# Performance work log

Measured on AMD Instinct MI355X. Metric: run time of the kernel, lower is better.

## Reference

```python
import jax, jax.numpy as jnp
import numpy as np
from math import sqrt

B, S, D, H = 4, 2048, 1024, 16
DH = D // H          # 64
DF = 4 * D           # 4096
EPS = 1e-5
NEG = -1e9


def layer_norm(x, w, b):
    mu = jnp.mean(x, axis=-1, keepdims=True)
    var = jnp.mean((x - mu) ** 2, axis=-1, keepdims=True)
    return (x - mu) * jax.lax.rsqrt(var + EPS) * w + b


def setup_inputs() -> dict:
    key = jax.random.key(0)
    ks = jax.random.split(key, 16)
    s = 0.02
    return {
        "state": jax.random.normal(ks[0], (B, S, D), jnp.float32),
        "mask": jax.random.randint(ks[1], (B, S), 0, 2, jnp.int32),
        "ln1_w": jnp.ones((D,), jnp.float32),
        "ln1_b": jnp.zeros((D,), jnp.float32),
        "Wq": jax.random.normal(ks[2], (H, D, DH), jnp.float32) * s,
        "bq": jnp.zeros((H, DH), jnp.float32),
        "Wk": jax.random.normal(ks[3], (H, D, DH), jnp.float32) * s,
        "bk": jnp.zeros((H, DH), jnp.float32),
        "Wv": jax.random.normal(ks[4], (H, D, DH), jnp.float32) * s,
        "bv": jnp.zeros((H, DH), jnp.float32),
        "Wo": jax.random.normal(ks[5], (D, D), jnp.float32) * s,
        "bo": jnp.zeros((D,), jnp.float32),
        "ln2_w": jnp.ones((D,), jnp.float32),
        "ln2_b": jnp.zeros((D,), jnp.float32),
        "W1": jax.random.normal(ks[6], (D, DF), jnp.float32) * s,
        "b1": jnp.zeros((DF,), jnp.float32),
        "W2": jax.random.normal(ks[7], (DF, D), jnp.float32) * s,
        "b2": jnp.zeros((D,), jnp.float32),
    }


def reference(state, mask, ln1_w, ln1_b, Wq, bq, Wk, bk, Wv, bv, Wo, bo,
              ln2_w, ln2_b, W1, b1, W2, b2):
    # pre-norm attention block
    hidden = layer_norm(state, ln1_w, ln1_b)               # [B,S,D]
    q = jnp.einsum("bsd,hde->bhse", hidden, Wq) + bq[None, :, None, :]
    k = jnp.einsum("bsd,hde->bhse", hidden, Wk) + bk[None, :, None, :]
    v = jnp.einsum("bsd,hde->bhse", hidden, Wv) + bv[None, :, None, :]
    scores = jnp.einsum("bhse,bhte->bhst", q, k) / sqrt(DH)  # [B,H,S,S]
    scores = jnp.where(mask[:, None, None, :] == 0, NEG, scores)
    weights = jax.nn.softmax(scores, axis=-1)
    attended = jnp.einsum("bhst,bhte->bhse", weights, v)    # [B,H,S,DH]
    # concat heads in head order (matches torch cat over per-head outputs)
    attended = attended.transpose(0, 2, 1, 3).reshape(B, S, D)
    attn_out = attended @ Wo + bo
    output = state + attn_out
    # pre-norm FFN block (dropout=0 -> identity)
    hidden = layer_norm(output, ln2_w, ln2_b)
    ff = jax.nn.gelu(hidden @ W1 + b1, approximate=False) @ W2 + b2
    return output + ff
```

## Files before the change

### kernel.cpp

```cpp
#include <hip/hip_runtime.h>
#include <math.h>

#define B_  4
#define S_  2048
#define D_  1024
#define H_  16
#define DH_ 64
#define DF_ 4096
#define M_  8192

#define QSC 0.18033688011112042f

typedef __attribute__((ext_vector_type(8))) short bf8_t;
typedef __attribute__((ext_vector_type(4))) float f4_t;

__device__ __forceinline__ unsigned short f2bf(float x) {
  union { float f; unsigned u; } v; v.f = x;
  unsigned r = v.u + 0x7fffu + ((v.u >> 16) & 1u);
  return (unsigned short)(r >> 16);
}

#if defined(__has_builtin)
#if __has_builtin(__builtin_amdgcn_cvt_pk_bf16_f32)
#define HAVE_PKCVT 1
#endif
#if __has_builtin(__builtin_amdgcn_global_load_lds)
#define HAVE_ASYNC 1
#endif
#endif

__device__ __forceinline__ unsigned pk_bf16(float lo, float hi) {
#ifdef HAVE_PKCVT
  auto r = __builtin_amdgcn_cvt_pk_bf16_f32(lo, hi);
  unsigned u; __builtin_memcpy(&u, &r, 4); return u;
#else
  return (unsigned)f2bf(lo) | ((unsigned)f2bf(hi) << 16);
#endif
}

__device__ __forceinline__ bf8_t upk8(unsigned u0, unsigned u1, unsigned u2, unsigned u3) {
  union { unsigned u[4]; bf8_t v; } c;
  c.u[0] = u0; c.u[1] = u1; c.u[2] = u2; c.u[3] = u3; return c.v;
}

__device__ __forceinline__ f4_t mfma32(bf8_t a, bf8_t b, f4_t c) {
  return __builtin_amdgcn_mfma_f32_16x16x32_bf16(a, b, c, 0, 0, 0);
}

__device__ __forceinline__ void async16(const void* g, void* l) {
#ifdef HAVE_ASYNC
  __builtin_amdgcn_global_load_lds((__attribute__((address_space(1))) void*)(g),
                                   (__attribute__((address_space(3))) void*)(l), 16, 0, 0);
#else
  *(uint4*)l = *(const uint4*)g;
#endif
}

__device__ __forceinline__ int sw(int row) { return (row ^ (row >> 3)) & 7; }


__global__ __launch_bounds__(256) void wtrans_kernel(const float* __restrict__ in,
                                                     unsigned short* __restrict__ out,
                                                     int K, int N) {
  const int k0 = blockIdx.x * 32, n0 = blockIdx.y * 32;
  __shared__ float t[32][33];
  const int tid = threadIdx.x;
#pragma unroll
  for (int i = 0; i < 4; i++) {
    int idx = i * 256 + tid; int r = idx >> 5, c = idx & 31;
    t[r][c] = in[(size_t)(k0 + r) * N + n0 + c];
  }
  __syncthreads();
#pragma unroll
  for (int i = 0; i < 4; i++) {
    int idx = i * 256 + tid; int r = idx >> 5, c = idx & 31;
    out[(size_t)(n0 + r) * K + k0 + c] = f2bf(t[c][r]);
  }
}

__global__ __launch_bounds__(256) void qkvpack_kernel(const float* __restrict__ Wq,
                                                      const float* __restrict__ Wk,
                                                      const float* __restrict__ Wv,
                                                      unsigned short* __restrict__ WqkvT) {
  const int z = blockIdx.z;
  const int sel = z >> 4, h = z & 15;
  const float* in = (sel == 0 ? Wq : sel == 1 ? Wk : Wv) + (size_t)h * D_ * DH_;
  const int k0 = blockIdx.x * 32, n0 = blockIdx.y * 32;
  __shared__ float t[32][33];
  const int tid = threadIdx.x;
#pragma unroll
  for (int i = 0; i < 4; i++) {
    int idx = i * 256 + tid; int r = idx >> 5, c = idx & 31;
    t[r][c] = in[(size_t)(k0 + r) * DH_ + n0 + c];
  }
  __syncthreads();
#pragma unroll
  for (int i = 0; i < 4; i++) {
    int idx = i * 256 + tid; int r = idx >> 5, c = idx & 31;
    int n = sel * 1024 + h * 64 + n0 + r;
    WqkvT[(size_t)n * D_ + k0 + c] = f2bf(t[c][r]);
  }
}

__global__ void biaspack_kernel(const float* __restrict__ bq, const float* __restrict__ bk,
                                const float* __restrict__ bv, float* __restrict__ bqkv) {
  int i = blockIdx.x * 256 + threadIdx.x;
  if (i < 3072) {
    int sel = i >> 10, j = i & 1023;
    const float* src = sel == 0 ? bq : sel == 1 ? bk : bv;
    bqkv[i] = src[j];
  }
}


__global__ __launch_bounds__(256) void ln_kernel(const float* __restrict__ x,
                                                 const float* __restrict__ w,
                                                 const float* __restrict__ bb,
                                                 unsigned short* __restrict__ out) {
  const int row = blockIdx.x;
  const float* xr = x + (size_t)row * D_;
  const int tid = threadIdx.x;
  float v[4]; float s = 0.f;
#pragma unroll
  for (int i = 0; i < 4; i++) { v[i] = xr[tid + i * 256]; s += v[i]; }
  __shared__ float red[8];
#pragma unroll
  for (int o = 32; o; o >>= 1) s += __shfl_xor(s, o, 64);
  const int wv = tid >> 6, ln = tid & 63;
  if (!ln) red[wv] = s;
  __syncthreads();
  float mean = (red[0] + red[1] + red[2] + red[3]) * (1.f / 1024.f);
  float s2 = 0.f;
#pragma unroll
  for (int i = 0; i < 4; i++) { float d = v[i] - mean; s2 += d * d; }
#pragma unroll
  for (int o = 32; o; o >>= 1) s2 += __shfl_xor(s2, o, 64);
  if (!ln) red[4 + wv] = s2;
  __syncthreads();
  float var = (red[4] + red[5] + red[6] + red[7]) * (1.f / 1024.f);
  float rstd = rsqrtf(var + 1e-5f);
#pragma unroll
  for (int i = 0; i < 4; i++) {
    int c = tid + i * 256;
    out[(size_t)row * D_ + c] = f2bf((v[i] - mean) * rstd * w[c] + bb[c]);
  }
}

template <int EPI>
__global__ __launch_bounds__(256) void gemm_bt(const unsigned short* __restrict__ A,
                                               const unsigned short* __restrict__ Bt,
                                               const float* __restrict__ bias,
                                               const float* __restrict__ resid,
                                               unsigned short* __restrict__ outb,
                                               float* __restrict__ outf,
                                               int Ndim, int Kdim) {
  __shared__ __align__(16) unsigned short Asmem[4096];
  __shared__ __align__(16) unsigned short Bsmem[4096];
  const int tid = threadIdx.x;
  const int wave = tid >> 6, lane = tid & 63;
  const int quad = lane >> 4, l16 = lane & 15;
  const int wm = wave >> 1, wn = wave & 1;
  const int m0 = blockIdx.y * 128, n0 = blockIdx.x * 128;

  const f4_t fzero = {0.f, 0.f, 0.f, 0.f};
  f4_t acc[4][4];
#pragma unroll
  for (int i = 0; i < 4; i++)
#pragma unroll
    for (int j = 0; j < 4; j++) acc[i][j] = fzero;

  const int rowA = tid >> 2;
  const int kp = (tid & 3) * 8;

  for (int k0 = 0; k0 < Kdim; k0 += 32) {
    __syncthreads();
#pragma unroll
    for (int r = 0; r < 2; r++) {
      const int row = r * 64 + rowA;
      const int e = row * 32 + kp;
      async16(A  + (size_t)(m0 + row) * Kdim + k0 + kp, &Asmem[e]);
      async16(Bt + (size_t)(n0 + row) * Kdim + k0 + kp, &Bsmem[e]);
    }
    __syncthreads();

    bf8_t a[4], b[4];
#pragma unroll
    for (int i = 0; i < 4; i++) {
      a[i] = *(const bf8_t*)&Asmem[(wm * 64 + i * 16 + l16) * 32 + quad * 8];
      b[i] = *(const bf8_t*)&Bsmem[(wn * 64 + i * 16 + l16) * 32 + quad * 8];
    }
#pragma unroll
    for (int i = 0; i < 4; i++)
#pragma unroll
      for (int j = 0; j < 4; j++)
        acc[i][j] = mfma32(a[i], b[j], acc[i][j]);
  }

  const float sc = (EPI == 0 && n0 < 1024) ? QSC : 1.f;
#pragma unroll
  for (int i = 0; i < 4; i++) {
#pragma unroll
    for (int j = 0; j < 4; j++) {
#pragma unroll
      for (int r = 0; r < 4; r++) {
        const int m = m0 + wm * 64 + i * 16 + quad * 4 + r;
        const int n = n0 + wn * 64 + j * 16 + l16;
        float v = acc[i][j][r] + bias[n];
        if constexpr (EPI == 0) v *= sc;
        if constexpr (EPI == 2) v = 0.5f * v * (1.f + erff(v * 0.70710678118654752f));
        if constexpr (EPI == 1) {
          v += resid[(size_t)m * Ndim + n];
          outf[(size_t)m * Ndim + n] = v;
        } else {
          outb[(size_t)m * Ndim + n] = f2bf(v);
        }
      }
    }
  }
}


__global__ __launch_bounds__(256) void vtrans_kernel(const unsigned short* __restrict__ qkv,
                                                     unsigned short* __restrict__ vT) {
  const int bh = blockIdx.y, b = bh >> 4, h = bh & 15;
  const int t0 = blockIdx.x * 64;
  __shared__ unsigned short tile[64][65];
  const int tid = threadIdx.x;
#pragma unroll
  for (int i = 0; i < 16; i++) {
    int idx = i * 256 + tid;
    int t = idx >> 6, e = idx & 63;
    tile[e][t] = qkv[(size_t)(b * S_ + t0 + t) * 3072 + 2048 + h * 64 + e];
  }
  __syncthreads();
#pragma unroll
  for (int i = 0; i < 16; i++) {
    int idx = i * 256 + tid;
    int e = idx >> 6, t = idx & 63;
    int gt = (t & 32) + 8 * ((t >> 2) & 3) + 4 * ((t >> 4) & 1) + (t & 3);
    vT[(size_t)(bh * 64 + e) * S_ + t0 + gt] = tile[e][t];
  }
}


__global__ __launch_bounds__(256) void attn_kernel(const unsigned short* __restrict__ qkv,
                                                   const unsigned short* __restrict__ vT,
                                                   const int* __restrict__ maskp,
                                                   unsigned short* __restrict__ attended) {
  const int bh = blockIdx.y, b = bh >> 4, h = bh & 15;
  const int q0 = blockIdx.x * 128;
  const int tid = threadIdx.x, wv = tid >> 6, lane = tid & 63;
  const int quad = lane >> 4, l16 = lane & 15;
  __shared__ __align__(16) unsigned short smem[9216];
  __shared__ float biasl[64];
  unsigned short* Ks = smem;
  unsigned short* Vs = smem + 4096;

  bf8_t aq[2][2];
#pragma unroll
  for (int sb = 0; sb < 2; sb++) {
    const unsigned short* qrow =
        qkv + (size_t)(b * S_ + q0 + wv * 32 + sb * 16 + l16) * 3072 + h * 64;
    aq[sb][0] = *(const bf8_t*)(qrow + quad * 8);
    aq[sb][1] = *(const bf8_t*)(qrow + 32 + quad * 8);
  }

  const bf8_t ones8 = {0x3F80, 0x3F80, 0x3F80, 0x3F80, 0x3F80, 0x3F80, 0x3F80, 0x3F80};
  const f4_t fzero = {0.f, 0.f, 0.f, 0.f};
  f4_t o[2][4], lacc[2];
#pragma unroll
  for (int sb = 0; sb < 2; sb++) {
    lacc[sb] = fzero;
#pragma unroll
    for (int ee = 0; ee < 4; ee++) o[sb][ee] = fzero;
  }

  for (int t0 = 0; t0 < S_; t0 += 64) {
    __syncthreads();
#pragma unroll
    for (int r = 0; r < 2; r++) {
      int ci = r * 256 + tid;
      int row = ci >> 3, lc = (ci & 7) ^ sw(row);
      async16(qkv + (size_t)(b * S_ + t0 + row) * 3072 + 1024 + h * 64 + lc * 8, &Ks[ci * 8]);
      async16(vT + (size_t)(bh * 64 + row) * S_ + t0 + lc * 8, &Vs[ci * 8]);
    }
    if (tid < 64) biasl[tid] = maskp[b * S_ + t0 + tid] ? 0.f : -8e9f;
    __syncthreads();

    f4_t sf[2][4];
#pragma unroll
    for (int jj = 0; jj < 4; jj++) {
      f4_t bi = *(const f4_t*)&biasl[jj * 16 + quad * 4];
      sf[0][jj] = bi;
      sf[1][jj] = bi;
    }
#pragma unroll
    for (int jj = 0; jj < 4; jj++) {
      int krow = jj * 16 + l16, sk = sw(krow);
      bf8_t kf0 = *(const bf8_t*)&Ks[krow * 64 + (quad ^ sk) * 8];
      bf8_t kf1 = *(const bf8_t*)&Ks[krow * 64 + ((quad + 4) ^ sk) * 8];
      sf[0][jj] = mfma32(kf0, aq[0][0], sf[0][jj]);
      sf[0][jj] = mfma32(kf1, aq[0][1], sf[0][jj]);
      sf[1][jj] = mfma32(kf0, aq[1][0], sf[1][jj]);
      sf[1][jj] = mfma32(kf1, aq[1][1], sf[1][jj]);
    }

    bf8_t pp[2][2];
#pragma unroll
    for (int sb = 0; sb < 2; sb++) {
#pragma unroll
      for (int h2 = 0; h2 < 2; h2++) {
        float p0 = exp2f(sf[sb][2 * h2][0]),     p1 = exp2f(sf[sb][2 * h2][1]);
        float p2 = exp2f(sf[sb][2 * h2][2]),     p3 = exp2f(sf[sb][2 * h2][3]);
        float p4 = exp2f(sf[sb][2 * h2 + 1][0]), p5 = exp2f(sf[sb][2 * h2 + 1][1]);
        float p6 = exp2f(sf[sb][2 * h2 + 1][2]), p7 = exp2f(sf[sb][2 * h2 + 1][3]);
        pp[sb][h2] = upk8(pk_bf16(p0, p1), pk_bf16(p2, p3),
                          pk_bf16(p4, p5), pk_bf16(p6, p7));
      }
      lacc[sb] = mfma32(ones8, pp[sb][0], lacc[sb]);
      lacc[sb] = mfma32(ones8, pp[sb][1], lacc[sb]);
    }

#pragma unroll
    for (int ee = 0; ee < 4; ee++) {
      int vrow = ee * 16 + l16, sv = sw(vrow);
#pragma unroll
      for (int h2 = 0; h2 < 2; h2++) {
        bf8_t vf = *(const bf8_t*)&Vs[vrow * 64 + ((4 * h2 + quad) ^ sv) * 8];
        o[0][ee] = mfma32(vf, pp[0][h2], o[0][ee]);
        o[1][ee] = mfma32(vf, pp[1][h2], o[1][ee]);
      }
    }
  }

  float linv[2];
#pragma unroll
  for (int sb = 0; sb < 2; sb++) linv[sb] = 1.f / lacc[sb][0];

  __syncthreads();
  unsigned short* Os = smem;
#pragma unroll
  for (int sb = 0; sb < 2; sb++) {
    int srow = wv * 32 + sb * 16 + l16;
#pragma unroll
    for (int ee = 0; ee < 4; ee++) {
      unsigned w0 = pk_bf16(o[sb][ee][0] * linv[sb], o[sb][ee][1] * linv[sb]);
      unsigned w1 = pk_bf16(o[sb][ee][2] * linv[sb], o[sb][ee][3] * linv[sb]);
      uint2 wq; wq.x = w0; wq.y = w1;
      *(uint2*)&Os[srow * 72 + ee * 16 + quad * 4] = wq;
    }
  }
  __syncthreads();
#pragma unroll
  for (int it = 0; it < 4; it++) {
    int row = it * 32 + (tid >> 3), e0 = (tid & 7) * 8;
    bf8_t v = *(const bf8_t*)&Os[row * 72 + e0];
    *(bf8_t*)&attended[(size_t)(b * S_ + q0 + row) * D_ + h * 64 + e0] = v;
  }
}


extern "C" void kernel_launch(void* const* d_in, const int* in_sizes, int n_in,
                              void* d_out, int out_size, void* d_ws, size_t ws_size,
                              hipStream_t stream) {
  const float* state = (const float*)d_in[0];
  const int*   maskp = (const int*)d_in[1];
  const float* ln1w  = (const float*)d_in[2];
  const float* ln1b  = (const float*)d_in[3];
  const float* Wq    = (const float*)d_in[4];
  const float* bq    = (const float*)d_in[5];
  const float* Wk    = (const float*)d_in[6];
  const float* bk    = (const float*)d_in[7];
  const float* Wv    = (const float*)d_in[8];
  const float* bv    = (const float*)d_in[9];
  const float* Wo    = (const float*)d_in[10];
  const float* bo    = (const float*)d_in[11];
  const float* ln2w  = (const float*)d_in[12];
  const float* ln2b  = (const float*)d_in[13];
  const float* W1    = (const float*)d_in[14];
  const float* b1    = (const float*)d_in[15];
  const float* W2    = (const float*)d_in[16];
  const float* b2    = (const float*)d_in[17];

  char* w = (char*)d_ws;
  unsigned short* hidden = (unsigned short*)w; w += (size_t)M_ * D_ * 2;
  unsigned short* qkv    = (unsigned short*)w; w += (size_t)M_ * 3072 * 2;
  unsigned short* vT     = (unsigned short*)w; w += (size_t)M_ * D_ * 2;
  float*          outp   = (float*)w;          w += (size_t)M_ * D_ * 4;
  unsigned short* WqkvT  = (unsigned short*)w; w += (size_t)3072 * D_ * 2;
  unsigned short* WoT    = (unsigned short*)w; w += (size_t)D_ * D_ * 2;
  unsigned short* W1T    = (unsigned short*)w; w += (size_t)DF_ * D_ * 2;
  unsigned short* W2T    = (unsigned short*)w; w += (size_t)D_ * DF_ * 2;
  float*          bqkv   = (float*)w;          w += 3072 * 4;
  unsigned short* ff1    = qkv;

  qkvpack_kernel<<<dim3(32, 2, 48), 256, 0, stream>>>(Wq, Wk, Wv, WqkvT);
  wtrans_kernel<<<dim3(32, 32), 256, 0, stream>>>(Wo, WoT, D_, D_);
  wtrans_kernel<<<dim3(32, 128), 256, 0, stream>>>(W1, W1T, D_, DF_);
  wtrans_kernel<<<dim3(128, 32), 256, 0, stream>>>(W2, W2T, DF_, D_);
  biaspack_kernel<<<12, 256, 0, stream>>>(bq, bk, bv, bqkv);

  ln_kernel<<<M_, 256, 0, stream>>>(state, ln1w, ln1b, hidden);
  gemm_bt<0><<<dim3(3072 / 128, M_ / 128), 256, 0, stream>>>(hidden, WqkvT, bqkv, nullptr,
                                                             qkv, nullptr, 3072, D_);
  vtrans_kernel<<<dim3(S_ / 64, B_ * H_), 256, 0, stream>>>(qkv, vT);
  attn_kernel<<<dim3(S_ / 128, B_ * H_), 256, 0, stream>>>(qkv, vT, maskp, hidden);
  gemm_bt<1><<<dim3(D_ / 128, M_ / 128), 256, 0, stream>>>(hidden, WoT, bo, state,
                                                           nullptr, outp, D_, D_);
  ln_kernel<<<M_, 256, 0, stream>>>(outp, ln2w, ln2b, hidden);
  gemm_bt<2><<<dim3(DF_ / 128, M_ / 128), 256, 0, stream>>>(hidden, W1T, b1, nullptr,
                                                            ff1, nullptr, DF_, D_);
  gemm_bt<1><<<dim3(D_ / 128, M_ / 128), 256, 0, stream>>>(ff1, W2T, b2, outp,
                                                           nullptr, (float*)d_out, D_, DF_);
}
```

Before: 655.1 us.

## Fuse V transpose into QKV GEMM epilogue and widen attention key tile

The QKV GEMM epilogue now writes the V columns straight into the transposed, permuted vT layout, so the separate vtrans kernel and its extra pass over V are removed. The attention kernel loads 128 keys per iteration instead of 64, processing two halves per barrier pair, which halves the synchronisation count at the cost of doubled LDS use. exp2f is replaced by the hardware exp2 builtin. The vT layout and swizzle had to be reworked to match the new load pattern, so index errors are the main risk.

```diff
diff --git a/kernel.cpp b/kernel.cpp
--- a/kernel.cpp
+++ b/kernel.cpp
@@ -14,12 +14,6 @@
 typedef __attribute__((ext_vector_type(8))) short bf8_t;
 typedef __attribute__((ext_vector_type(4))) float f4_t;
 
-__device__ __forceinline__ unsigned short f2bf(float x) {
-  union { float f; unsigned u; } v; v.f = x;
-  unsigned r = v.u + 0x7fffu + ((v.u >> 16) & 1u);
-  return (unsigned short)(r >> 16);
-}
-
 #if defined(__has_builtin)
 #if __has_builtin(__builtin_amdgcn_cvt_pk_bf16_f32)
 #define HAVE_PKCVT 1
@@ -27,6 +21,13 @@
 #if __has_builtin(__builtin_amdgcn_global_load_lds)
 #define HAVE_ASYNC 1
 #endif
+#if __has_builtin(__builtin_amdgcn_exp2f)
+#define EXP2F(x) __builtin_amdgcn_exp2f(x)
+#else
+#define EXP2F(x) __expf((x) * 0.69314718055994531f)
+#endif
+#else
+#define EXP2F(x) __expf((x) * 0.69314718055994531f)
 #endif
 
 __device__ __forceinline__ unsigned pk_bf16(float lo, float hi) {
@@ -34,8 +35,15 @@
   auto r = __builtin_amdgcn_cvt_pk_bf16_f32(lo, hi);
   unsigned u; __builtin_memcpy(&u, &r, 4); return u;
 #else
-  return (unsigned)f2bf(lo) | ((unsigned)f2bf(hi) << 16);
-#endif
+  union { float f; unsigned u; } a, b2; a.f = lo; b2.f = hi;
+  unsigned ra = a.u + 0x7fffu + ((a.u >> 16) & 1u);
+  unsigned rb = b2.u + 0x7fffu + ((b2.u >> 16) & 1u);
+  return (ra >> 16) | (rb & 0xffff0000u);
+#endif
+}
+
+__device__ __forceinline__ unsigned short f2bf(float x) {
+  return (unsigned short)(pk_bf16(x, x) & 0xffffu);
 }
 
 __device__ __forceinline__ bf8_t upk8(unsigned u0, unsigned u1, unsigned u2, unsigned u3) {
@@ -153,6 +161,7 @@
                                                const float* __restrict__ resid,
                                                unsigned short* __restrict__ outb,
                                                float* __restrict__ outf,
+                                               unsigned short* __restrict__ vTout,
                                                int Ndim, int Kdim) {
   __shared__ __align__(16) unsigned short Asmem[4096];
   __shared__ __align__(16) unsigned short Bsmem[4096];
@@ -194,6 +203,27 @@
 #pragma unroll
       for (int j = 0; j < 4; j++)
         acc[i][j] = mfma32(a[i], b[j], acc[i][j]);
+  }
+
+  if (EPI == 0 && n0 >= 2048) {
+    const int bb2 = m0 >> 11;
+    const int s_base = (m0 & 2047) + wm * 64;
+#pragma unroll
+    for (int i = 0; i < 4; i++) {
+      const int g0 = (i & 2) * 16 + 8 * quad + 4 * (i & 1);
+#pragma unroll
+      for (int j = 0; j < 4; j++) {
+        const int n = n0 + wn * 64 + j * 16 + l16;
+        const int ef = n - 2048;
+        const int hh = ef >> 6, e = ef & 63;
+        const float bsv = bias[n];
+        uint2 wq;
+        wq.x = pk_bf16(acc[i][j][0] + bsv, acc[i][j][1] + bsv);
+        wq.y = pk_bf16(acc[i][j][2] + bsv, acc[i][j][3] + bsv);
+        *(uint2*)&vTout[(size_t)((bb2 * 16 + hh) * 64 + e) * S_ + s_base + g0] = wq;
+      }
+    }
+    return;
   }
 
   const float sc = (EPI == 0 && n0 < 1024) ? QSC : 1.f;
@@ -220,29 +250,6 @@
 }
 
 
-__global__ __launch_bounds__(256) void vtrans_kernel(const unsigned short* __restrict__ qkv,
-                                                     unsigned short* __restrict__ vT) {
-  const int bh = blockIdx.y, b = bh >> 4, h = bh & 15;
-  const int t0 = blockIdx.x * 64;
-  __shared__ unsigned short tile[64][65];
-  const int tid = threadIdx.x;
-#pragma unroll
-  for (int i = 0; i < 16; i++) {
-    int idx = i * 256 + tid;
-    int t = idx >> 6, e = idx & 63;
-    tile[e][t] = qkv[(size_t)(b * S_ + t0 + t) * 3072 + 2048 + h * 64 + e];
-  }
-  __syncthreads();
-#pragma unroll
-  for (int i = 0; i < 16; i++) {
-    int idx = i * 256 + tid;
-    int e = idx >> 6, t = idx & 63;
-    int gt = (t & 32) + 8 * ((t >> 2) & 3) + 4 * ((t >> 4) & 1) + (t & 3);
-    vT[(size_t)(bh * 64 + e) * S_ + t0 + gt] = tile[e][t];
-  }
-}
-
-
 __global__ __launch_bounds__(256) void attn_kernel(const unsigned short* __restrict__ qkv,
                                                    const unsigned short* __restrict__ vT,
                                                    const int* __restrict__ maskp,
@@ -251,10 +258,10 @@
   const int q0 = blockIdx.x * 128;
   const int tid = threadIdx.x, wv = tid >> 6, lane = tid & 63;
   const int quad = lane >> 4, l16 = lane & 15;
-  __shared__ __align__(16) unsigned short smem[9216];
-  __shared__ float biasl[64];
+  __shared__ __align__(16) unsigned short smem[16384];
+  __shared__ float biasl[128];
   unsigned short* Ks = smem;
-  unsigned short* Vs = smem + 4096;
+  unsigned short* Vs = smem + 8192;
 
   bf8_t aq[2][2];
 #pragma unroll
@@ -275,60 +282,66 @@
     for (int ee = 0; ee < 4; ee++) o[sb][ee] = fzero;
   }
 
-  for (int t0 = 0; t0 < S_; t0 += 64) {
+  for (int t0 = 0; t0 < S_; t0 += 128) {
     __syncthreads();
 #pragma unroll
-    for (int r = 0; r < 2; r++) {
+    for (int r = 0; r < 4; r++) {
       int ci = r * 256 + tid;
-      int row = ci >> 3, lc = (ci & 7) ^ sw(row);
-      async16(qkv + (size_t)(b * S_ + t0 + row) * 3072 + 1024 + h * 64 + lc * 8, &Ks[ci * 8]);
-      async16(vT + (size_t)(bh * 64 + row) * S_ + t0 + lc * 8, &Vs[ci * 8]);
-    }
-    if (tid < 64) biasl[tid] = maskp[b * S_ + t0 + tid] ? 0.f : -8e9f;
+      int krow = ci >> 3, kc = (ci & 7) ^ sw(krow);
+      async16(qkv + (size_t)(b * S_ + t0 + krow) * 3072 + 1024 + h * 64 + kc * 8,
+              &Ks[ci * 8]);
+      int e = ci >> 4, half = (ci >> 3) & 1, vc = (ci & 7) ^ sw(e);
+      async16(vT + (size_t)(bh * 64 + e) * S_ + t0 + half * 64 + vc * 8,
+              &Vs[ci * 8]);
+    }
+    if (tid < 128) biasl[tid] = maskp[b * S_ + t0 + tid] ? 0.f : -8e9f;
     __syncthreads();
 
-    f4_t sf[2][4];
-#pragma unroll
-    for (int jj = 0; jj < 4; jj++) {
-      f4_t bi = *(const f4_t*)&biasl[jj * 16 + quad * 4];
-      sf[0][jj] = bi;
-      sf[1][jj] = bi;
-    }
-#pragma unroll
-    for (int jj = 0; jj < 4; jj++) {
-      int krow = jj * 16 + l16, sk = sw(krow);
-      bf8_t kf0 = *(const bf8_t*)&Ks[krow * 64 + (quad ^ sk) * 8];
-      bf8_t kf1 = *(const bf8_t*)&Ks[krow * 64 + ((quad + 4) ^ sk) * 8];
-      sf[0][jj] = mfma32(kf0, aq[0][0], sf[0][jj]);
-      sf[0][jj] = mfma32(kf1, aq[0][1], sf[0][jj]);
-      sf[1][jj] = mfma32(kf0, aq[1][0], sf[1][jj]);
-      sf[1][jj] = mfma32(kf1, aq[1][1], sf[1][jj]);
-    }
-
-    bf8_t pp[2][2];
-#pragma unroll
-    for (int sb = 0; sb < 2; sb++) {
-#pragma unroll
-      for (int h2 = 0; h2 < 2; h2++) {
-        float p0 = exp2f(sf[sb][2 * h2][0]),     p1 = exp2f(sf[sb][2 * h2][1]);
-        float p2 = exp2f(sf[sb][2 * h2][2]),     p3 = exp2f(sf[sb][2 * h2][3]);
-        float p4 = exp2f(sf[sb][2 * h2 + 1][0]), p5 = exp2f(sf[sb][2 * h2 + 1][1]);
-        float p6 = exp2f(sf[sb][2 * h2 + 1][2]), p7 = exp2f(sf[sb][2 * h2 + 1][3]);
-        pp[sb][h2] = upk8(pk_bf16(p0, p1), pk_bf16(p2, p3),
-                          pk_bf16(p4, p5), pk_bf16(p6, p7));
-      }
-      lacc[sb] = mfma32(ones8, pp[sb][0], lacc[sb]);
-      lacc[sb] = mfma32(ones8, pp[sb][1], lacc[sb]);
-    }
-
-#pragma unroll
-    for (int ee = 0; ee < 4; ee++) {
-      int vrow = ee * 16 + l16, sv = sw(vrow);
-#pragma unroll
-      for (int h2 = 0; h2 < 2; h2++) {
-        bf8_t vf = *(const bf8_t*)&Vs[vrow * 64 + ((4 * h2 + quad) ^ sv) * 8];
-        o[0][ee] = mfma32(vf, pp[0][h2], o[0][ee]);
-        o[1][ee] = mfma32(vf, pp[1][h2], o[1][ee]);
+#pragma unroll
+    for (int th = 0; th < 2; th++) {
+      f4_t sf[2][4];
+#pragma unroll
+      for (int jj = 0; jj < 4; jj++) {
+        f4_t bi = *(const f4_t*)&biasl[th * 64 + jj * 16 + quad * 4];
+        sf[0][jj] = bi;
+        sf[1][jj] = bi;
+      }
+#pragma unroll
+      for (int jj = 0; jj < 4; jj++) {
+        int krow = th * 64 + jj * 16 + l16, sk = sw(krow);
+        bf8_t kf0 = *(const bf8_t*)&Ks[krow * 64 + (quad ^ sk) * 8];
+        bf8_t kf1 = *(const bf8_t*)&Ks[krow * 64 + ((quad + 4) ^ sk) * 8];
+        sf[0][jj] = mfma32(kf0, aq[0][0], sf[0][jj]);
+        sf[0][jj] = mfma32(kf1, aq[0][1], sf[0][jj]);
+        sf[1][jj] = mfma32(kf0, aq[1][0], sf[1][jj]);
+        sf[1][jj] = mfma32(kf1, aq[1][1], sf[1][jj]);
+      }
+
+      bf8_t pp[2][2];
+#pragma unroll
+      for (int sb = 0; sb < 2; sb++) {
+#pragma unroll
+        for (int h2 = 0; h2 < 2; h2++) {
+          float p0 = EXP2F(sf[sb][2 * h2][0]),     p1 = EXP2F(sf[sb][2 * h2][1]);
+          float p2 = EXP2F(sf[sb][2 * h2][2]),     p3 = EXP2F(sf[sb][2 * h2][3]);
+          float p4 = EXP2F(sf[sb][2 * h2 + 1][0]), p5 = EXP2F(sf[sb][2 * h2 + 1][1]);
+          float p6 = EXP2F(sf[sb][2 * h2 + 1][2]), p7 = EXP2F(sf[sb][2 * h2 + 1][3]);
+          pp[sb][h2] = upk8(pk_bf16(p0, p1), pk_bf16(p2, p3),
+                            pk_bf16(p4, p5), pk_bf16(p6, p7));
+        }
+        lacc[sb] = mfma32(ones8, pp[sb][0], lacc[sb]);
+        lacc[sb] = mfma32(ones8, pp[sb][1], lacc[sb]);
+      }
+
+#pragma unroll
+      for (int ee = 0; ee < 4; ee++) {
+        int vrow = ee * 16 + l16, sv = sw(vrow);
+#pragma unroll
+        for (int h2 = 0; h2 < 2; h2++) {
+          bf8_t vf = *(const bf8_t*)&Vs[vrow * 128 + th * 64 + ((4 * h2 + quad) ^ sv) * 8];
+          o[0][ee] = mfma32(vf, pp[0][h2], o[0][ee]);
+          o[1][ee] = mfma32(vf, pp[1][h2], o[1][ee]);
+        }
       }
     }
   }
@@ -402,14 +415,13 @@
 
   ln_kernel<<<M_, 256, 0, stream>>>(state, ln1w, ln1b, hidden);
   gemm_bt<0><<<dim3(3072 / 128, M_ / 128), 256, 0, stream>>>(hidden, WqkvT, bqkv, nullptr,
-                                                             qkv, nullptr, 3072, D_);
-  vtrans_kernel<<<dim3(S_ / 64, B_ * H_), 256, 0, stream>>>(qkv, vT);
+                                                             qkv, nullptr, vT, 3072, D_);
   attn_kernel<<<dim3(S_ / 128, B_ * H_), 256, 0, stream>>>(qkv, vT, maskp, hidden);
   gemm_bt<1><<<dim3(D_ / 128, M_ / 128), 256, 0, stream>>>(hidden, WoT, bo, state,
-                                                           nullptr, outp, D_, D_);
+                                                           nullptr, outp, nullptr, D_, D_);
   ln_kernel<<<M_, 256, 0, stream>>>(outp, ln2w, ln2b, hidden);
   gemm_bt<2><<<dim3(DF_ / 128, M_ / 128), 256, 0, stream>>>(hidden, W1T, b1, nullptr,
-                                                            ff1, nullptr, DF_, D_);
+                                                            ff1, nullptr, nullptr, DF_, D_);
   gemm_bt<1><<<dim3(D_ / 128, M_ / 128), 256, 0, stream>>>(ff1, W2T, b2, outp,
-                                                           nullptr, (float*)d_out, D_, DF_);
-}
+                                                           nullptr, (float*)d_out, nullptr, D_, DF_);
+}
```

Measured after the change: 613.4 us. -6.4%, faster.
